# Performance work log

Measured on AMD Instinct MI355X. Metric: run time of the kernel, lower is better.

Reference implementation:

```python
import jax, jax.numpy as jnp
import numpy as np

EPS_BN = 1e-5
EPS_W = 1e-8


def setup_inputs() -> dict:
    key = jax.random.key(0)
    ks = jax.random.split(key, 6)
    B, N, S, D1, D2 = 8, 8192, 2048, 128, 256
    Cin = D1 + D2  # 384
    return {
        "points_position": jax.random.normal(ks[0], (B, 3, N), jnp.float32),
        "sampled_points_position": jax.random.normal(ks[1], (B, 3, S), jnp.float32),
        "skip_points_feature": jax.random.normal(ks[2], (B, D1, N), jnp.float32),
        "sampled_points_feature": jax.random.normal(ks[3], (B, D2, S), jnp.float32),
        "W1": jax.random.normal(ks[4], (256, Cin), jnp.float32) * 0.05,
        "b1": jnp.zeros((256,), jnp.float32),
        "g1": jnp.ones((256,), jnp.float32),
        "beta1": jnp.zeros((256,), jnp.float32),
        "W2": jax.random.normal(ks[5], (128, 256), jnp.float32) * 0.05,
        "b2": jnp.zeros((128,), jnp.float32),
        "g2": jnp.ones((128,), jnp.float32),
        "beta2": jnp.zeros((128,), jnp.float32),
    }


def _bn_relu(x, g, b):
    # train-mode BatchNorm1d over (batch, points) per channel, x: [B,N,C]
    mean = jnp.mean(x, axis=(0, 1), keepdims=True)
    var = jnp.mean(jnp.square(x - mean), axis=(0, 1), keepdims=True)  # biased var
    return jax.nn.relu((x - mean) * jax.lax.rsqrt(var + EPS_BN) * g + b)


def reference(points_position, sampled_points_position, skip_points_feature,
              sampled_points_feature, W1, b1, g1, beta1, W2, b2, g2, beta2):
    pos = points_position.transpose(0, 2, 1)            # [B,N,3]
    spos = sampled_points_position.transpose(0, 2, 1)   # [B,S,3]
    sfeat = sampled_points_feature.transpose(0, 2, 1)   # [B,S,D2]

    # squared pairwise distance [B,N,S]
    d = (jnp.sum(pos * pos, axis=-1, keepdims=True)
         - 2.0 * jnp.einsum("bnc,bsc->bns", pos, spos)
         + jnp.sum(spos * spos, axis=-1)[:, None, :])

    # 3 nearest neighbors (smallest distances)
    neg_d3, idx = jax.lax.top_k(-d, 3)                  # [B,N,3]
    d3 = -neg_d3
    w = 1.0 / (d3 + EPS_W)
    w = w / jnp.sum(w, axis=-1, keepdims=True)          # [B,N,3]

    gathered = jax.vmap(lambda f, i: f[i])(sfeat, idx)  # [B,N,3,D2]
    interp = jnp.einsum("bnk,bnkd->bnd", w, gathered)   # [B,N,D2]

    feat = jnp.concatenate([skip_points_feature.transpose(0, 2, 1), interp], axis=-1)  # [B,N,D1+D2]

    h = _bn_relu(jnp.einsum("bnc,oc->bno", feat, W1) + b1, g1, beta1)  # [B,N,256]
    h = _bn_relu(jnp.einsum("bnc,oc->bno", h, W2) + b2, g2, beta2)     # [B,N,128]
    return h.transpose(0, 2, 1)                          # [B,128,N]
```

## Files before the change

kernel.cpp:

```cpp
#include <hip/hip_runtime.h>

constexpr int BATCH = 8;
constexpr int NPT   = 8192;
constexpr int NSMP  = 2048;
constexpr int D1C   = 128;
constexpr int D2C   = 256;
constexpr int CIN   = 384;
constexpr int C1    = 256;
constexpr int C2    = 128;
constexpr int BN_TOTAL = BATCH * NPT;

constexpr int BM = 128, BK = 32;
constexpr int NRB = BN_TOTAL / BM;

typedef __bf16 bf16x8 __attribute__((ext_vector_type(8)));
typedef short  s16x8  __attribute__((ext_vector_type(8)));
typedef float  f32x4  __attribute__((ext_vector_type(4)));
typedef unsigned short u16x4 __attribute__((ext_vector_type(4)));

__device__ __forceinline__ unsigned short f2bf(float x) {
  unsigned u = __builtin_bit_cast(unsigned, x);
  u += 0x7fffu + ((u >> 16) & 1u);
  return (unsigned short)(u >> 16);
}
__device__ __forceinline__ float bf2f(unsigned short h) {
  return __builtin_bit_cast(float, (unsigned)h << 16);
}

__device__ __forceinline__ void gld_lds16(const void* g, void* l) {
  __builtin_amdgcn_global_load_lds(
      (const __attribute__((address_space(1))) void*)g,
      (__attribute__((address_space(3))) void*)l, 16, 0, 0);
}

constexpr int PT_T = (NSMP / 32) * (D2C / 32) * BATCH;
constexpr int PT_S = (NPT / 32) * (D1C / 32) * BATCH;
constexpr int PT_M = (C1 * CIN + 255) / 256;

__global__ __launch_bounds__(256) void prep_all(
    const float* __restrict__ sfeat, float* __restrict__ sfeatT,
    const float* __restrict__ skip, unsigned short* __restrict__ featB,
    const float* __restrict__ spos, float* __restrict__ sposI,
    float4* __restrict__ qs4,
    const float* __restrict__ W1, unsigned short* __restrict__ W1h,
    const float* __restrict__ W2, unsigned short* __restrict__ W2h,
    float* __restrict__ stats) {
  __shared__ float tile[32][33];
  int bid = blockIdx.x, tid = threadIdx.x;
  int tx = tid & 31, ty = tid >> 5;
  if (bid < PT_T) {
    int z = bid >> 9;
    int r = bid & 511;
    int c0 = (r & 63) * 32;
    int r0 = (r >> 6) * 32;
    const float* inb = sfeat + (size_t)z * D2C * NSMP;
    float* outb = sfeatT + (size_t)z * NSMP * D2C;
#pragma unroll
    for (int i = 0; i < 32; i += 8)
      tile[ty + i][tx] = inb[(size_t)(r0 + ty + i) * NSMP + c0 + tx];
    __syncthreads();
#pragma unroll
    for (int i = 0; i < 32; i += 8)
      outb[(size_t)(c0 + ty + i) * D2C + r0 + tx] = tile[tx][ty + i];
  } else if (bid < PT_T + PT_S) {
    int id = bid - PT_T;
    int z = id >> 10;
    int r = id & 1023;
    int n0 = (r & 255) * 32;
    int d0 = (r >> 8) * 32;
#pragma unroll
    for (int i = 0; i < 32; i += 8)
      tile[ty + i][tx] = skip[((size_t)z * D1C + d0 + ty + i) * NPT + n0 + tx];
    __syncthreads();
#pragma unroll
    for (int i = 0; i < 32; i += 8) {
      int n = n0 + ty + i;
      featB[((size_t)z * NPT + n) * CIN + d0 + tx] = f2bf(tile[tx][ty + i]);
    }
  } else {
    int g = (bid - PT_T - PT_S) * 256 + tid;
    if (g < 768) stats[g] = 0.f;
    if (g < C1 * CIN) W1h[g] = f2bf(W1[g]);
    if (g < C2 * C1)  W2h[g] = f2bf(W2[g]);
    if (g < BATCH * NSMP) {
      int b = g >> 11, s = g & (NSMP - 1);
      const float* sp = spos + (size_t)b * 3 * NSMP;
      float x = sp[s], y = sp[NSMP + s], z = sp[2 * NSMP + s];
      sposI[(size_t)g * 3 + 0] = x;
      sposI[(size_t)g * 3 + 1] = y;
      sposI[(size_t)g * 3 + 2] = z;
      qs4[g] = make_float4(-2.f * x, -2.f * y, -2.f * z,
                           fmaf(x, x, fmaf(y, y, z * z)));
    }
  }
}

constexpr int KWAVES = 8;
constexpr int SEGK = NSMP / KWAVES;

__device__ __forceinline__ void ins_med3(float kf, float& k0, float& k1,
                                         float& k2, float& k3) {
  float o0 = k0, o1 = k1, o2 = k2;
  k0 = fminf(kf, o0);
  k1 = __builtin_amdgcn_fmed3f(kf, o0, o1);
  k2 = __builtin_amdgcn_fmed3f(kf, o1, o2);
  k3 = __builtin_amdgcn_fmed3f(kf, o2, k3);
}

__global__ __launch_bounds__(512, 2) void knn_scan(
    const float* __restrict__ pos,
    const float4* __restrict__ qs4g,
    float* __restrict__ mkG) {
  __shared__ __align__(16) float4 qs[NSMP];

  int tid = threadIdx.x;
  int wave = tid >> 6, lane = tid & 63;
  int blk = blockIdx.x;
  int b = blk & 7;
  int n0 = (blk >> 3) << 8;

  const float* pb = pos + (size_t)b * 3 * NPT;
  float px[4], py[4], pz[4], pp[4];
#pragma unroll
  for (int m = 0; m < 4; m++) {
    int n = n0 + (m << 6) + lane;
    px[m] = pb[n]; py[m] = pb[NPT + n]; pz[m] = pb[2 * NPT + n];
    pp[m] = fmaf(px[m], px[m], fmaf(py[m], py[m], pz[m] * pz[m]));
  }

  const float INF = __builtin_inff();
  float k0[4], k1[4], k2[4], k3[4];
#pragma unroll
  for (int m = 0; m < 4; m++) { k0[m] = INF; k1[m] = INF; k2[m] = INF; k3[m] = INF; }

  int s0 = wave * SEGK;
  const float4* qsrc = qs4g + (size_t)b * NSMP;
#pragma unroll
  for (int r = 0; r < 4; r++)
    gld_lds16(&qsrc[s0 + r * 64 + lane], &qs[s0 + r * 64]);
  __syncthreads();

#define KSTEP4(Q, SS)                                                        \
  {                                                                          \
    _Pragma("unroll")                                                        \
    for (int m_ = 0; m_ < 4; m_++) {                                         \
      float tt = (Q).w + pp[m_];       \
      float d_ = fmaf(px[m_], (Q).x,                                         \
                      fmaf(py[m_], (Q).y, fmaf(pz[m_], (Q).z, tt)));         \
      unsigned ki_ = (__builtin_bit_cast(unsigned, d_) & 0xFFFFF800u) |      \
                     (unsigned)(SS);                                         \
      ins_med3(__builtin_bit_cast(float, ki_), k0[m_], k1[m_], k2[m_], k3[m_]); \
    }                                                                        \
  }

  for (int t = 0; t < SEGK; t += 8) {
    float4 qv[8];
#pragma unroll
    for (int u = 0; u < 8; u++) qv[u] = qs[s0 + t + u];
#pragma unroll
    for (int u = 0; u < 8; u++) KSTEP4(qv[u], s0 + t + u)
  }
#undef KSTEP4

  size_t gbase = (size_t)b * NPT + n0 + lane;
#pragma unroll
  for (int m = 0; m < 4; m++) {
    size_t gp = gbase + (m << 6);
    mkG[(size_t)(wave * 4 + 0) * BN_TOTAL + gp] = k0[m];
    mkG[(size_t)(wave * 4 + 1) * BN_TOTAL + gp] = k1[m];
    mkG[(size_t)(wave * 4 + 2) * BN_TOTAL + gp] = k2[m];
    mkG[(size_t)(wave * 4 + 3) * BN_TOTAL + gp] = k3[m];
  }
}

__device__ __forceinline__ bool dless(double d, int i, double D, int I) {
  return d < D || (d == D && i < I);
}
__device__ __forceinline__ void dins3(double d, int i,
                                      double& b0, double& b1, double& b2,
                                      int& i0, int& i1, int& i2) {
  if (dless(d, i, b2, i2)) {
    if (dless(d, i, b1, i1)) {
      b2 = b1; i2 = i1;
      if (dless(d, i, b0, i0)) { b1 = b0; i1 = i0; b0 = d; i0 = i; }
      else                     { b1 = d; i1 = i; }
    } else { b2 = d; i2 = i; }
  }
}

constexpr int PPB_P = 64;

__global__ __launch_bounds__(256) void knn_post(
    const float* __restrict__ pos,
    const float* __restrict__ sposI,
    const float* __restrict__ mkG,
    const float* __restrict__ sfeatT,
    unsigned short* __restrict__ featB) {
  __shared__ int   il[PPB_P][3];
  __shared__ float wl[PPB_P][3];
  __shared__ int   fl[PPB_P];
  __shared__ int   fcnt;

  int tid = threadIdx.x;
  int wave = tid >> 6, lane = tid & 63;
  int blk = blockIdx.x;
  int b = blk & 7;
  int n0 = (blk >> 3) * PPB_P;

  if (tid == 0) fcnt = 0;
  __syncthreads();

  const float* pb = pos + (size_t)b * 3 * NPT;
  const float INF = __builtin_inff();

  if (tid < PPB_P) {
    size_t gp = (size_t)b * NPT + n0 + tid;
    float K0 = INF, K1 = INF, K2 = INF, K3 = INF;
#pragma unroll
    for (int pl = 0; pl < 32; pl++)
      ins_med3(mkG[(size_t)pl * BN_TOTAL + gp], K0, K1, K2, K3);

    int I0 = (int)(__builtin_bit_cast(unsigned, K0) & 0x7FFu);
    int I1 = (int)(__builtin_bit_cast(unsigned, K1) & 0x7FFu);
    int I2 = (int)(__builtin_bit_cast(unsigned, K2) & 0x7FFu);
    float d2m = __builtin_bit_cast(float, __builtin_bit_cast(unsigned, K2) & 0xFFFFF800u);
    float d3m = __builtin_bit_cast(float, __builtin_bit_cast(unsigned, K3) & 0xFFFFF800u);
    bool flag = (d3m - d2m) < 2e-3f * fmaxf(d3m, 0.f) + 1e-5f;
    if (flag) {
      int slot = atomicAdd(&fcnt, 1);
      fl[slot] = tid;
    }
    int n = n0 + tid;
    const float* q = sposI + (size_t)b * 3 * NSMP;
    double pxd = (double)pb[n], pyd = (double)pb[NPT + n], pzd = (double)pb[2 * NPT + n];
    double dd[3]; int II[3] = {I0, I1, I2};
#pragma unroll
    for (int k = 0; k < 3; k++) {
      double dx = pxd - (double)q[3 * II[k]];
      double dy = pyd - (double)q[3 * II[k] + 1];
      double dz = pzd - (double)q[3 * II[k] + 2];
      dd[k] = dx * dx + dy * dy + dz * dz;
    }
    double w0 = 1.0 / (dd[0] + 1e-8);
    double w1 = 1.0 / (dd[1] + 1e-8);
    double w2 = 1.0 / (dd[2] + 1e-8);
    double inv = 1.0 / (w0 + w1 + w2);
    il[tid][0] = I0; il[tid][1] = I1; il[tid][2] = I2;
    wl[tid][0] = (float)(w0 * inv);
    wl[tid][1] = (float)(w1 * inv);
    wl[tid][2] = (float)(w2 * inv);
  }
  __syncthreads();

  int fc = fcnt;
  for (int t = wave; t < fc; t += 4) {
    int P = fl[t];
    int n = n0 + P;
    double pxd = (double)pb[n], pyd = (double)pb[NPT + n], pzd = (double)pb[2 * NPT + n];
    const float* q = sposI + (size_t)b * 3 * NSMP;
    double b0 = 1e300, b1 = 1e300, b2 = 1e300;
    int i0 = 0x7FFFFFFF, i1 = 0x7FFFFFFF, i2 = 0x7FFFFFFF;
    for (int s = lane; s < NSMP; s += 64) {
      double dx = pxd - (double)q[3 * s];
      double dy = pyd - (double)q[3 * s + 1];
      double dz = pzd - (double)q[3 * s + 2];
      double d = dx * dx + dy * dy + dz * dz;
      dins3(d, s, b0, b1, b2, i0, i1, i2);
    }
#pragma unroll
    for (int m = 1; m < 64; m <<= 1) {
      double o0 = __shfl_xor(b0, m, 64), o1 = __shfl_xor(b1, m, 64), o2 = __shfl_xor(b2, m, 64);
      int    j0 = __shfl_xor(i0, m, 64), j1 = __shfl_xor(i1, m, 64), j2 = __shfl_xor(i2, m, 64);
      dins3(o0, j0, b0, b1, b2, i0, i1, i2);
      dins3(o1, j1, b0, b1, b2, i0, i1, i2);
      dins3(o2, j2, b0, b1, b2, i0, i1, i2);
    }
    if (lane == 0) {
      double w0 = 1.0 / (b0 + 1e-8);
      double w1 = 1.0 / (b1 + 1e-8);
      double w2 = 1.0 / (b2 + 1e-8);
      double inv = 1.0 / (w0 + w1 + w2);
      il[P][0] = i0; il[P][1] = i1; il[P][2] = i2;
      wl[P][0] = (float)(w0 * inv);
      wl[P][1] = (float)(w1 * inv);
      wl[P][2] = (float)(w2 * inv);
    }
  }
  __syncthreads();

  const float* base = sfeatT + (size_t)b * NSMP * D2C;
  for (int i = 0; i < 16; i++) {
    int P = (wave << 4) + i;
    int i0 = il[P][0], i1 = il[P][1], i2 = il[P][2];
    float w0 = wl[P][0], w1 = wl[P][1], w2 = wl[P][2];
    float4 v0 = *(const float4*)&base[(size_t)i0 * D2C + (lane << 2)];
    float4 v1 = *(const float4*)&base[(size_t)i1 * D2C + (lane << 2)];
    float4 v2 = *(const float4*)&base[(size_t)i2 * D2C + (lane << 2)];
    u16x4 o;
    o[0] = f2bf(w0 * v0.x + w1 * v1.x + w2 * v2.x);
    o[1] = f2bf(w0 * v0.y + w1 * v1.y + w2 * v2.y);
    o[2] = f2bf(w0 * v0.z + w1 * v1.z + w2 * v2.z);
    o[3] = f2bf(w0 * v0.w + w1 * v1.w + w2 * v2.w);
    *(u16x4*)&featB[((size_t)b * NPT + n0 + P) * CIN + D1C + (lane << 2)] = o;
  }
}

__global__ __launch_bounds__(256) void gemm1_mw(
    const unsigned short* __restrict__ featB,
    const unsigned short* __restrict__ W1h,
    const float* __restrict__ bias,
    unsigned short* __restrict__ Y1,
    float* __restrict__ sum1,
    float* __restrict__ sumsq1) {
  __shared__ __align__(16) unsigned short As[BM * BK];
  __shared__ __align__(16) unsigned short Bs[BM * BK];
  int tid = threadIdx.x;
  int lane = tid & 63, w = tid >> 6;
  int wr = w >> 1, wc = w & 1;
  int m16 = lane & 15, quad = lane >> 4;
  int cb = blockIdx.x, rb = blockIdx.y;
  int row0 = rb * BM, col0 = cb * BM;
  int srow = lane >> 2, scol8 = (lane & 3) * 8;

  f32x4 acc[4][4];
#pragma unroll
  for (int j = 0; j < 4; j++) {
    float bj = bias[col0 + wc * 64 + j * 16 + m16];
#pragma unroll
    for (int i = 0; i < 4; i++) acc[i][j] = f32x4{bj, bj, bj, bj};
  }

  for (int k0 = 0; k0 < CIN; k0 += BK) {
#pragma unroll
    for (int kq = 0; kq < 2; kq++) {
      int ar = 32 * w + 16 * kq + srow;
      int lb = __builtin_amdgcn_readfirstlane((32 * w + 16 * kq) * BK);
      gld_lds16(&featB[(size_t)(row0 + ar) * CIN + k0 + scol8], &As[lb]);
      gld_lds16(&W1h[(size_t)(col0 + ar) * CIN + k0 + scol8], &Bs[lb]);
    }
    __syncthreads();

    bf16x8 a[4], bb[4];
#pragma unroll
    for (int i = 0; i < 4; i++)
      a[i] = __builtin_bit_cast(bf16x8,
          *(const s16x8*)&As[(wr * 64 + i * 16 + m16) * BK + quad * 8]);
#pragma unroll
    for (int j = 0; j < 4; j++)
      bb[j] = __builtin_bit_cast(bf16x8,
          *(const s16x8*)&Bs[(wc * 64 + j * 16 + m16) * BK + quad * 8]);
#pragma unroll
    for (int i = 0; i < 4; i++)
#pragma unroll
      for (int j = 0; j < 4; j++)
        acc[i][j] = __builtin_amdgcn_mfma_f32_16x16x32_bf16(a[i], bb[j], acc[i][j], 0, 0, 0);
    __syncthreads();
  }

#pragma unroll
  for (int j = 0; j < 4; j++) {
    int col = col0 + wc * 64 + j * 16 + m16;
    float s = 0.f, q = 0.f;
#pragma unroll
    for (int i = 0; i < 4; i++)
#pragma unroll
      for (int r = 0; r < 4; r++) {
        float v = acc[i][j][r];
        Y1[(size_t)(row0 + wr * 64 + i * 16 + quad * 4 + r) * C1 + col] = f2bf(v);
        s += v; q = fmaf(v, v, q);
      }
    s += __shfl_xor(s, 16, 64); s += __shfl_xor(s, 32, 64);
    q += __shfl_xor(q, 16, 64); q += __shfl_xor(q, 32, 64);
    if (quad == 0) {
      atomicAdd(&sum1[col], s);
      atomicAdd(&sumsq1[col], q);
    }
  }
}

__global__ __launch_bounds__(256) void gemm2_mw(
    const unsigned short* __restrict__ Y1,
    const float* __restrict__ g1, const float* __restrict__ beta1,
    const float* __restrict__ sum1, const float* __restrict__ sumsq1,
    const unsigned short* __restrict__ W2h,
    const float* __restrict__ bias,
    unsigned short* __restrict__ Y2,
    float* __restrict__ sum2, float* __restrict__ sumsq2) {
  __shared__ __align__(16) unsigned short As[BM * BK];
  __shared__ __align__(16) unsigned short Bs[BM * BK];
  __shared__ float scs[C1], shs[C1];
  int tid = threadIdx.x;
  int lane = tid & 63, w = tid >> 6;
  int wr = w >> 1, wc = w & 1;
  int m16 = lane & 15, quad = lane >> 4;
  int rb = blockIdx.x;
  int row0 = rb * BM, col0 = 0;
  int srow = lane >> 2, scol8 = (lane & 3) * 8;

  {
    const float invBN = 1.0f / (float)BN_TOTAL;
    float mean = sum1[tid] * invBN;
    float var = sumsq1[tid] * invBN - mean * mean;
    float sc = g1[tid] / sqrtf(var + 1e-5f);
    scs[tid] = sc;
    shs[tid] = beta1[tid] - mean * sc;
  }

  f32x4 acc[4][4];
#pragma unroll
  for (int j = 0; j < 4; j++) {
    float bj = bias[col0 + wc * 64 + j * 16 + m16];
#pragma unroll
    for (int i = 0; i < 4; i++) acc[i][j] = f32x4{bj, bj, bj, bj};
  }
  __syncthreads();

  for (int k0 = 0; k0 < C1; k0 += BK) {
#pragma unroll
    for (int kq = 0; kq < 2; kq++) {
      int ar = 32 * w + 16 * kq + srow;
      int lb = __builtin_amdgcn_readfirstlane((32 * w + 16 * kq) * BK);
      gld_lds16(&W2h[(size_t)(col0 + ar) * C1 + k0 + scol8], &Bs[lb]);
      s16x8 v = *(const s16x8*)&Y1[(size_t)(row0 + ar) * C1 + k0 + scol8];
      unsigned short ov[8];
#pragma unroll
      for (int e = 0; e < 8; e++) {
        float x = bf2f((unsigned short)v[e]);
        float y = fmaxf(fmaf(x, scs[k0 + scol8 + e], shs[k0 + scol8 + e]), 0.f);
        ov[e] = f2bf(y);
      }
      *(s16x8*)&As[ar * BK + scol8] = *(const s16x8*)ov;
    }
    __syncthreads();

    bf16x8 a[4], bb[4];
#pragma unroll
    for (int i = 0; i < 4; i++)
      a[i] = __builtin_bit_cast(bf16x8,
          *(const s16x8*)&As[(wr * 64 + i * 16 + m16) * BK + quad * 8]);
#pragma unroll
    for (int j = 0; j < 4; j++)
      bb[j] = __builtin_bit_cast(bf16x8,
          *(const s16x8*)&Bs[(wc * 64 + j * 16 + m16) * BK + quad * 8]);
#pragma unroll
    for (int i = 0; i < 4; i++)
#pragma unroll
      for (int j = 0; j < 4; j++)
        acc[i][j] = __builtin_amdgcn_mfma_f32_16x16x32_bf16(a[i], bb[j], acc[i][j], 0, 0, 0);
    __syncthreads();
  }

#pragma unroll
  for (int j = 0; j < 4; j++) {
    int col = col0 + wc * 64 + j * 16 + m16;
    float s = 0.f, q = 0.f;
#pragma unroll
    for (int i = 0; i < 4; i++)
#pragma unroll
      for (int r = 0; r < 4; r++) {
        float v = acc[i][j][r];
        Y2[(size_t)(row0 + wr * 64 + i * 16 + quad * 4 + r) * C2 + col] = f2bf(v);
        s += v; q = fmaf(v, v, q);
      }
    s += __shfl_xor(s, 16, 64); s += __shfl_xor(s, 32, 64);
    q += __shfl_xor(q, 16, 64); q += __shfl_xor(q, 32, 64);
    if (quad == 0) {
      atomicAdd(&sum2[col], s);
      atomicAdd(&sumsq2[col], q);
    }
  }
}

__global__ void final_kernel(const unsigned short* __restrict__ Y2,
                             const float* __restrict__ sum2,
                             const float* __restrict__ sumsq2,
                             const float* __restrict__ g2,
                             const float* __restrict__ beta2,
                             float* __restrict__ out) {
  __shared__ float tile[32][33];
  int b = blockIdx.z;
  int n0 = blockIdx.x * 32;
  int c0 = blockIdx.y * 32;
  int tx = threadIdx.x, ty = threadIdx.y;
  int c = c0 + tx;
  const float invBN = 1.0f / (float)BN_TOTAL;
  float mean = sum2[c] * invBN;
  float var = sumsq2[c] * invBN - mean * mean;
  float sc = g2[c] / sqrtf(var + 1e-5f);
  float sh = beta2[c] - mean * sc;
#pragma unroll
  for (int i = 0; i < 32; i += 8) {
    int n = n0 + ty + i;
    float v = bf2f(Y2[((size_t)b * NPT + n) * C2 + c0 + tx]);
    tile[ty + i][tx] = fmaxf(fmaf(v, sc, sh), 0.f);
  }
  __syncthreads();
#pragma unroll
  for (int i = 0; i < 32; i += 8) {
    int cc = c0 + ty + i;
    out[((size_t)b * C2 + cc) * NPT + n0 + tx] = tile[tx][ty + i];
  }
}

extern "C" void kernel_launch(void* const* d_in, const int* in_sizes, int n_in,
                              void* d_out, int out_size, void* d_ws, size_t ws_size,
                              hipStream_t stream) {
  (void)in_sizes; (void)n_in; (void)out_size; (void)ws_size;
  const float* pos   = (const float*)d_in[0];
  const float* spos  = (const float*)d_in[1];
  const float* skip  = (const float*)d_in[2];
  const float* sfeat = (const float*)d_in[3];
  const float* W1    = (const float*)d_in[4];
  const float* b1    = (const float*)d_in[5];
  const float* g1    = (const float*)d_in[6];
  const float* beta1 = (const float*)d_in[7];
  const float* W2    = (const float*)d_in[8];
  const float* b2    = (const float*)d_in[9];
  const float* g2    = (const float*)d_in[10];
  const float* beta2 = (const float*)d_in[11];
  float* out = (float*)d_out;

  float* ws = (float*)d_ws;
  size_t off = 0;
  float* sfeatT  = ws + off; off += (size_t)BATCH * NSMP * D2C;
  unsigned short* featB = (unsigned short*)(ws + off); off += (size_t)BN_TOTAL * CIN / 2;
  unsigned short* Y1    = (unsigned short*)(ws + off); off += (size_t)BN_TOTAL * C1 / 2;
  unsigned short* Y2    = (unsigned short*)(ws + off); off += (size_t)BN_TOTAL * C2 / 2;
  unsigned short* W1h   = (unsigned short*)(ws + off); off += (size_t)C1 * CIN / 2;
  unsigned short* W2h   = (unsigned short*)(ws + off); off += (size_t)C2 * C1 / 2;
  float* sposI   = ws + off; off += (size_t)BATCH * NSMP * 3;
  float4* qs4    = (float4*)(ws + off); off += (size_t)BATCH * NSMP * 4;
  float* mkG     = ws + off; off += (size_t)32 * BN_TOTAL;
  float* stats   = ws + off; off += 1024;
  float* sum1   = stats;
  float* sumsq1 = stats + 256;
  float* sum2   = stats + 512;
  float* sumsq2 = stats + 640;

  prep_all<<<PT_T + PT_S + PT_M, 256, 0, stream>>>(
      sfeat, sfeatT, skip, featB, spos, sposI, qs4, W1, W1h, W2, W2h, stats);

  knn_scan<<<BN_TOTAL / 256, 512, 0, stream>>>(pos, qs4, mkG);

  knn_post<<<BN_TOTAL / PPB_P, 256, 0, stream>>>(pos, sposI, mkG, sfeatT, featB);

  gemm1_mw<<<dim3(C1 / BM, NRB), 256, 0, stream>>>(
      featB, W1h, b1, Y1, sum1, sumsq1);

  gemm2_mw<<<NRB, 256, 0, stream>>>(
      Y1, g1, beta1, sum1, sumsq1, W2h, b2, Y2, sum2, sumsq2);

  final_kernel<<<dim3(NPT / 32, C2 / 32, BATCH), dim3(32, 8), 0, stream>>>(
      Y2, sum2, sumsq2, g2, beta2, out);
}
```

Measured before the change: 303.5 us.

## Parallelize knn_post merge, unroll gather, double-buffer full-width gemm1 tiles

Result: no change. 305.2 us (+0.5%).

```diff
diff --git a/kernel.cpp b/kernel.cpp
--- a/kernel.cpp
+++ b/kernel.cpp
@@ -190,12 +190,13 @@
 
 constexpr int PPB_P = 64;
 
-__global__ __launch_bounds__(256) void knn_post(
+__global__ __launch_bounds__(256, 4) void knn_post(
     const float* __restrict__ pos,
     const float* __restrict__ sposI,
     const float* __restrict__ mkG,
     const float* __restrict__ sfeatT,
     unsigned short* __restrict__ featB) {
+  __shared__ float pm[4][4][64];
   __shared__ int   il[PPB_P][3];
   __shared__ float wl[PPB_P][3];
   __shared__ int   fl[PPB_P];
@@ -208,17 +209,37 @@
   int n0 = (blk >> 3) * PPB_P;
 
   if (tid == 0) fcnt = 0;
-  __syncthreads();
 
   const float* pb = pos + (size_t)b * 3 * NPT;
   const float INF = __builtin_inff();
 
+  {
+    size_t gp = (size_t)b * NPT + n0 + lane;
+    float v0 = mkG[(size_t)(wave * 8 + 0) * BN_TOTAL + gp];
+    float v1 = mkG[(size_t)(wave * 8 + 1) * BN_TOTAL + gp];
+    float v2 = mkG[(size_t)(wave * 8 + 2) * BN_TOTAL + gp];
+    float v3 = mkG[(size_t)(wave * 8 + 3) * BN_TOTAL + gp];
+    float v4 = mkG[(size_t)(wave * 8 + 4) * BN_TOTAL + gp];
+    float v5 = mkG[(size_t)(wave * 8 + 5) * BN_TOTAL + gp];
+    float v6 = mkG[(size_t)(wave * 8 + 6) * BN_TOTAL + gp];
+    float v7 = mkG[(size_t)(wave * 8 + 7) * BN_TOTAL + gp];
+    float K0 = INF, K1 = INF, K2 = INF, K3 = INF;
+    ins_med3(v0, K0, K1, K2, K3); ins_med3(v1, K0, K1, K2, K3);
+    ins_med3(v2, K0, K1, K2, K3); ins_med3(v3, K0, K1, K2, K3);
+    ins_med3(v4, K0, K1, K2, K3); ins_med3(v5, K0, K1, K2, K3);
+    ins_med3(v6, K0, K1, K2, K3); ins_med3(v7, K0, K1, K2, K3);
+    pm[wave][0][lane] = K0; pm[wave][1][lane] = K1;
+    pm[wave][2][lane] = K2; pm[wave][3][lane] = K3;
+  }
+  __syncthreads();
+
   if (tid < PPB_P) {
-    size_t gp = (size_t)b * NPT + n0 + tid;
     float K0 = INF, K1 = INF, K2 = INF, K3 = INF;
 #pragma unroll
-    for (int pl = 0; pl < 32; pl++)
-      ins_med3(mkG[(size_t)pl * BN_TOTAL + gp], K0, K1, K2, K3);
+    for (int w = 0; w < 4; w++)
+#pragma unroll
+      for (int sl = 0; sl < 4; sl++)
+        ins_med3(pm[w][sl][tid], K0, K1, K2, K3);
 
     int I0 = (int)(__builtin_bit_cast(unsigned, K0) & 0x7FFu);
     int I1 = (int)(__builtin_bit_cast(unsigned, K1) & 0x7FFu);
@@ -289,77 +310,109 @@
   __syncthreads();
 
   const float* base = sfeatT + (size_t)b * NSMP * D2C;
-  for (int i = 0; i < 16; i++) {
-    int P = (wave << 4) + i;
-    int i0 = il[P][0], i1 = il[P][1], i2 = il[P][2];
-    float w0 = wl[P][0], w1 = wl[P][1], w2 = wl[P][2];
-    float4 v0 = *(const float4*)&base[(size_t)i0 * D2C + (lane << 2)];
-    float4 v1 = *(const float4*)&base[(size_t)i1 * D2C + (lane << 2)];
-    float4 v2 = *(const float4*)&base[(size_t)i2 * D2C + (lane << 2)];
-    u16x4 o;
-    o[0] = f2bf(w0 * v0.x + w1 * v1.x + w2 * v2.x);
-    o[1] = f2bf(w0 * v0.y + w1 * v1.y + w2 * v2.y);
-    o[2] = f2bf(w0 * v0.z + w1 * v1.z + w2 * v2.z);
-    o[3] = f2bf(w0 * v0.w + w1 * v1.w + w2 * v2.w);
-    *(u16x4*)&featB[((size_t)b * NPT + n0 + P) * CIN + D1C + (lane << 2)] = o;
-  }
-}
-
-__global__ __launch_bounds__(256) void gemm1_mw(
+  for (int i = 0; i < 16; i += 2) {
+    int P0 = (wave << 4) + i, P1 = P0 + 1;
+    int a0 = il[P0][0], a1 = il[P0][1], a2 = il[P0][2];
+    int c0 = il[P1][0], c1 = il[P1][1], c2 = il[P1][2];
+    float aw0 = wl[P0][0], aw1 = wl[P0][1], aw2 = wl[P0][2];
+    float cw0 = wl[P1][0], cw1 = wl[P1][1], cw2 = wl[P1][2];
+    float4 u0 = *(const float4*)&base[(size_t)a0 * D2C + (lane << 2)];
+    float4 u1 = *(const float4*)&base[(size_t)a1 * D2C + (lane << 2)];
+    float4 u2 = *(const float4*)&base[(size_t)a2 * D2C + (lane << 2)];
+    float4 v0 = *(const float4*)&base[(size_t)c0 * D2C + (lane << 2)];
+    float4 v1 = *(const float4*)&base[(size_t)c1 * D2C + (lane << 2)];
+    float4 v2 = *(const float4*)&base[(size_t)c2 * D2C + (lane << 2)];
+    u16x4 o0, o1;
+    o0[0] = f2bf(aw0 * u0.x + aw1 * u1.x + aw2 * u2.x);
+    o0[1] = f2bf(aw0 * u0.y + aw1 * u1.y + aw2 * u2.y);
+    o0[2] = f2bf(aw0 * u0.z + aw1 * u1.z + aw2 * u2.z);
+    o0[3] = f2bf(aw0 * u0.w + aw1 * u1.w + aw2 * u2.w);
+    o1[0] = f2bf(cw0 * v0.x + cw1 * v1.x + cw2 * v2.x);
+    o1[1] = f2bf(cw0 * v0.y + cw1 * v1.y + cw2 * v2.y);
+    o1[2] = f2bf(cw0 * v0.z + cw1 * v1.z + cw2 * v2.z);
+    o1[3] = f2bf(cw0 * v0.w + cw1 * v1.w + cw2 * v2.w);
+    *(u16x4*)&featB[((size_t)b * NPT + n0 + P0) * CIN + D1C + (lane << 2)] = o0;
+    *(u16x4*)&featB[((size_t)b * NPT + n0 + P1) * CIN + D1C + (lane << 2)] = o1;
+  }
+}
+
+__global__ __launch_bounds__(512) void gemm1_mw(
     const unsigned short* __restrict__ featB,
     const unsigned short* __restrict__ W1h,
     const float* __restrict__ bias,
     unsigned short* __restrict__ Y1,
     float* __restrict__ sum1,
     float* __restrict__ sumsq1) {
-  __shared__ __align__(16) unsigned short As[BM * BK];
-  __shared__ __align__(16) unsigned short Bs[BM * BK];
+  __shared__ __align__(16) unsigned short As[2][BM * BK];
+  __shared__ __align__(16) unsigned short Bs[2][C1 * BK];
   int tid = threadIdx.x;
   int lane = tid & 63, w = tid >> 6;
-  int wr = w >> 1, wc = w & 1;
+  int wr = w >> 2, wc = w & 3;
   int m16 = lane & 15, quad = lane >> 4;
-  int cb = blockIdx.x, rb = blockIdx.y;
-  int row0 = rb * BM, col0 = cb * BM;
+  int rb = blockIdx.x;
+  int row0 = rb * BM;
   int srow = lane >> 2, scol8 = (lane & 3) * 8;
 
   f32x4 acc[4][4];
 #pragma unroll
   for (int j = 0; j < 4; j++) {
-    float bj = bias[col0 + wc * 64 + j * 16 + m16];
+    float bj = bias[wc * 64 + j * 16 + m16];
 #pragma unroll
     for (int i = 0; i < 4; i++) acc[i][j] = f32x4{bj, bj, bj, bj};
   }
 
-  for (int k0 = 0; k0 < CIN; k0 += BK) {
-#pragma unroll
-    for (int kq = 0; kq < 2; kq++) {
-      int ar = 32 * w + 16 * kq + srow;
-      int lb = __builtin_amdgcn_readfirstlane((32 * w + 16 * kq) * BK);
-      gld_lds16(&featB[(size_t)(row0 + ar) * CIN + k0 + scol8], &As[lb]);
-      gld_lds16(&W1h[(size_t)(col0 + ar) * CIN + k0 + scol8], &Bs[lb]);
-    }
-    __syncthreads();
-
-    bf16x8 a[4], bb[4];
-#pragma unroll
-    for (int i = 0; i < 4; i++)
-      a[i] = __builtin_bit_cast(bf16x8,
-          *(const s16x8*)&As[(wr * 64 + i * 16 + m16) * BK + quad * 8]);
-#pragma unroll
-    for (int j = 0; j < 4; j++)
-      bb[j] = __builtin_bit_cast(bf16x8,
-          *(const s16x8*)&Bs[(wc * 64 + j * 16 + m16) * BK + quad * 8]);
-#pragma unroll
-    for (int i = 0; i < 4; i++)
-#pragma unroll
-      for (int j = 0; j < 4; j++)
-        acc[i][j] = __builtin_amdgcn_mfma_f32_16x16x32_bf16(a[i], bb[j], acc[i][j], 0, 0, 0);
-    __syncthreads();
-  }
+#define STAGE1(buf, k0)                                                       \
+  {                                                                           \
+    int lbA = __builtin_amdgcn_readfirstlane((w * 16) * BK);                  \
+    gld_lds16(&featB[(size_t)(row0 + w * 16 + srow) * CIN + (k0) + scol8],    \
+              &As[buf][lbA]);                                                 \
+    int lb0 = __builtin_amdgcn_readfirstlane((w * 16) * BK);                  \
+    gld_lds16(&W1h[(size_t)(w * 16 + srow) * CIN + (k0) + scol8],             \
+              &Bs[buf][lb0]);                                                 \
+    int lb1 = __builtin_amdgcn_readfirstlane((128 + w * 16) * BK);            \
+    gld_lds16(&W1h[(size_t)(128 + w * 16 + srow) * CIN + (k0) + scol8],       \
+              &Bs[buf][lb1]);                                                 \
+  }
+
+#define COMPUTE1(buf)                                                         \
+  {                                                                           \
+    bf16x8 a[4], bb[4];                                                       \
+    _Pragma("unroll")                                                         \
+    for (int i = 0; i < 4; i++)                                               \
+      a[i] = __builtin_bit_cast(bf16x8,                                       \
+          *(const s16x8*)&As[buf][(wr * 64 + i * 16 + m16) * BK + quad * 8]); \
+    _Pragma("unroll")                                                         \
+    for (int j = 0; j < 4; j++)                                               \
+      bb[j] = __builtin_bit_cast(bf16x8,                                      \
+          *(const s16x8*)&Bs[buf][(wc * 64 + j * 16 + m16) * BK + quad * 8]); \
+    _Pragma("unroll")                                                         \
+    for (int i = 0; i < 4; i++)                                               \
+      _Pragma("unroll")                                                       \
+      for (int j = 0; j < 4; j++)                                             \
+        acc[i][j] = __builtin_amdgcn_mfma_f32_16x16x32_bf16(a[i], bb[j],      \
+                                                            acc[i][j], 0, 0, 0); \
+  }
+
+  STAGE1(0, 0)
+  int cur = 0;
+  for (int kt = 0; kt < CIN / BK - 1; ++kt) {
+    STAGE1(cur ^ 1, (kt + 1) * BK)
+    asm volatile("s_waitcnt vmcnt(3)" ::: "memory");
+    __builtin_amdgcn_s_barrier();
+    COMPUTE1(cur)
+    asm volatile("s_waitcnt lgkmcnt(0)" ::: "memory");
+    __builtin_amdgcn_s_barrier();
+    cur ^= 1;
+  }
+  asm volatile("s_waitcnt vmcnt(0)" ::: "memory");
+  __builtin_amdgcn_s_barrier();
+  COMPUTE1(cur)
+#undef STAGE1
+#undef COMPUTE1
 
 #pragma unroll
   for (int j = 0; j < 4; j++) {
-    int col = col0 + wc * 64 + j * 16 + m16;
+    int col = wc * 64 + j * 16 + m16;
     float s = 0.f, q = 0.f;
 #pragma unroll
     for (int i = 0; i < 4; i++)
@@ -544,8 +597,7 @@
 
   knn_post<<<BN_TOTAL / PPB_P, 256, 0, stream>>>(pos, sposI, mkG, sfeatT, featB);
 
-  gemm1_mw<<<dim3(C1 / BM, NRB), 256, 0, stream>>>(
-      featB, W1h, b1, Y1, sum1, sumsq1);
+  gemm1_mw<<<NRB, 512, 0, stream>>>(featB, W1h, b1, Y1, sum1, sumsq1);
 
   gemm2_mw<<<NRB, 256, 0, stream>>>(
       Y1, g1, beta1, sum1, sumsq1, W2h, b2, Y2, sum2, sumsq2);
```
